# Optimization experiments

Hardware: AMD Instinct MI355X
Metric: run time of the kernel (lower is better)

The kernel has to match this reference:

```python
import jax, jax.numpy as jnp
import numpy as np

B, S, D = 2, 2048, 1024
H, DH = 16, 64
BS = 512            # block_size
MAX_LEN = 2048      # rope base = max_seq_length
NB = S // BS        # number of blocks (no padding: S % BS == 0)


def setup_inputs() -> dict:
    key = jax.random.key(0)
    ks = jax.random.split(key, 5)
    s = 1.0 / np.sqrt(D)
    x = jax.random.normal(ks[0], (B, S, D), jnp.float32)
    Wq = jax.random.normal(ks[1], (D, D), jnp.float32) * s
    Wk = jax.random.normal(ks[2], (D, D), jnp.float32) * s
    Wv = jax.random.normal(ks[3], (D, D), jnp.float32) * s
    Wo = jax.random.normal(ks[4], (D, D), jnp.float32) * s
    z = jnp.zeros((D,), jnp.float32)
    return {"x": x, "Wq": Wq, "bq": z, "Wk": Wk, "bk": z,
            "Wv": Wv, "bv": z, "Wo": Wo, "bo": z}


def _apply_rope(q, k):
    # inv_freq uses max_seq_length as the base (as in the source module)
    inv_freq = 1.0 / MAX_LEN ** (jnp.arange(0, DH, 2, dtype=jnp.float32) / DH)  # [DH/2]
    pos = jnp.arange(S, dtype=jnp.float32)
    freqs = jnp.outer(pos, inv_freq)                 # [S, DH/2]
    cos = jnp.cos(freqs)[None, :, None, :]           # [1,S,1,DH/2]
    sin = jnp.sin(freqs)[None, :, None, :]
    half = DH // 2
    q1, q2 = q[..., :half], q[..., half:]
    k1, k2 = k[..., :half], k[..., half:]
    q_rot = jnp.concatenate([q1 * cos - q2 * sin, q1 * sin + q2 * cos], axis=-1)
    k_rot = jnp.concatenate([k1 * cos - k2 * sin, k1 * sin + k2 * cos], axis=-1)
    return q_rot, k_rot


def _block_attn(qb, q_start, kb, vb, k_start):
    # qb,kb,vb: [B,H,BS,DH]; returns attended [B,H,BS,DH], lse [B,H,BS]
    scale = 1.0 / jnp.sqrt(DH)
    scores = jnp.einsum('bhqd,bhkd->bhqk', qb, kb) * scale
    q_pos = jnp.arange(BS) + q_start
    k_pos = jnp.arange(BS) + k_start
    mask = (q_pos[:, None] >= k_pos[None, :])[None, None]   # [1,1,BS,BS]
    scores = jnp.where(mask, scores, -1e9)
    mx = jnp.max(scores, axis=-1, keepdims=True)
    mx = jnp.where(jnp.isinf(mx), 0.0, mx)
    e = jnp.where(mask, jnp.exp(scores - mx), 0.0)
    se = jnp.sum(e, axis=-1, keepdims=True) + 1e-10
    attended = jnp.einsum('bhqk,bhkd->bhqd', e / se, vb)
    lse = (jnp.log(se) + mx)[..., 0]                        # [B,H,BS]
    return attended, lse


def _forward(x, Wq, bq, Wk, bk, Wv, bv, Wo, bo):
    q = (x @ Wq + bq).reshape(B, S, H, DH)
    k = (x @ Wk + bk).reshape(B, S, H, DH)
    v = (x @ Wv + bv).reshape(B, S, H, DH)
    q, k = _apply_rope(q, k)
    # split into blocks: [NB, B, H, BS, DH]
    def to_blocks(t):
        return t.reshape(B, NB, BS, H, DH).transpose(1, 0, 3, 2, 4)
    qb, kb, vb = to_blocks(q), to_blocks(k), to_blocks(v)
    starts = jnp.arange(NB) * BS
    inner = jax.vmap(_block_attn, in_axes=(None, None, 0, 0, 0))   # over k blocks
    outer = jax.vmap(inner, in_axes=(0, 0, None, None, None))      # over q blocks
    att, lse = outer(qb, starts, kb, vb, starts)
    # att: [NBq,NBk,B,H,BS,DH], lse: [NBq,NBk,B,H,BS]
    mlse = jnp.max(lse, axis=1, keepdims=True)
    w = jnp.exp(lse - mlse)
    w = w / (jnp.sum(w, axis=1, keepdims=True) + 1e-10)
    acc = jnp.sum(att * w[..., None], axis=1)                      # [NBq,B,H,BS,DH]
    out = acc.transpose(1, 0, 3, 2, 4).reshape(B, S, D)
    out = out @ Wo + bo
    return out


def reference(x, Wq, bq, Wk, bk, Wv, bv, Wo, bo):
    out = _forward(x, Wq, bq, Wk, bk, Wv, bv, Wo, bo)
    attention_weights = jnp.ones((B, H, S, S), jnp.float32)  # dummy, as in source
    return out, attention_weights
```

## Files before the change

kernel.cpp:

```cpp
#include <hip/hip_runtime.h>
#include <cstdint>
#include <cstddef>

#define DEVINL __device__ __forceinline__

typedef float   f32x4  __attribute__((ext_vector_type(4)));
typedef float   vf4    __attribute__((ext_vector_type(4)));
typedef __bf16  bf16x8 __attribute__((ext_vector_type(8)));
typedef uint32_t u32;
typedef unsigned short u16;
typedef uint32_t u32x4 __attribute__((ext_vector_type(4)));

constexpr int Bb = 2, Ss = 2048, Dd = 1024, Hh = 16;
constexpr int Mm = Bb * Ss;


DEVINL u16 f2bf(float f) {
  union { float f; u32 u; } a; a.f = f;
  u32 r = a.u + 0x7fffu + ((a.u >> 16) & 1u);
  return (u16)(r >> 16);
}

typedef const __attribute__((address_space(1))) void* gas_t;
typedef __attribute__((address_space(3))) void* las_t;
DEVINL void gld_lds16(const void* g, void* l) {
  __builtin_amdgcn_global_load_lds((gas_t)g, (las_t)l, 16, 0, 0);
}

__global__ void fill_ones(vf4* __restrict__ p, long long n4) {
  size_t i = (size_t)blockIdx.x * blockDim.x + threadIdx.x;
  size_t stride = (size_t)gridDim.x * blockDim.x;
  const vf4 one = {1.f, 1.f, 1.f, 1.f};
  for (; i < (size_t)n4; i += stride)
    __builtin_nontemporal_store(one, p + i);
}

__global__ void rope_table(float* __restrict__ cosT, float* __restrict__ sinT) {
  int idx = blockIdx.x * 256 + threadIdx.x;
  int s = idx >> 5, j = idx & 31;
  float freq = (float)s * exp2f(-11.0f * (float)j / 32.0f);
  cosT[idx] = cosf(freq);
  sinT[idx] = sinf(freq);
}

__global__ void cast_x(const float* __restrict__ x, u16* __restrict__ xb) {
  size_t i = ((size_t)blockIdx.x * 256 + threadIdx.x) * 4;
  vf4 v = *(const vf4*)(x + i);
  union { u16 u[4]; unsigned long long q; } o;
  o.u[0] = f2bf(v.x); o.u[1] = f2bf(v.y); o.u[2] = f2bf(v.z); o.u[3] = f2bf(v.w);
  *(unsigned long long*)(xb + i) = o.q;
}

__global__ void transpose_cast_W(const float* __restrict__ W0, const float* __restrict__ W1,
                                 const float* __restrict__ W2, const float* __restrict__ W3,
                                 u16* __restrict__ Wt) {
  __shared__ u16 tile[64][72];
  const int z = blockIdx.z;
  const float* W = (z == 0) ? W0 : (z == 1) ? W1 : (z == 2) ? W2 : W3;
  u16* Out = Wt + (size_t)z * (Dd * Dd);
  const int k0 = blockIdx.x * 64, n0 = blockIdx.y * 64;
  const int tid = threadIdx.x;
#pragma unroll
  for (int it = 0; it < 4; ++it) {
    int r = it * 16 + (tid >> 4);
    int c = (tid & 15) * 4;
    vf4 v = *(const vf4*)(W + (size_t)(k0 + r) * Dd + n0 + c);
    tile[r][c + 0] = f2bf(v.x); tile[r][c + 1] = f2bf(v.y);
    tile[r][c + 2] = f2bf(v.z); tile[r][c + 3] = f2bf(v.w);
  }
  __syncthreads();
#pragma unroll
  for (int it = 0; it < 2; ++it) {
    int c = it * 256 + tid;
    int n = c >> 3, ck = c & 7;
    union { u16 u[8]; u32x4 q; } o;
#pragma unroll
    for (int j = 0; j < 8; ++j) o.u[j] = tile[ck * 8 + j][n];
    *(u32x4*)(Out + (size_t)(n0 + n) * Dd + k0 + ck * 8) = o.q;
  }
}

DEVINL void gemm_mainloop(const u16* __restrict__ A, const u16* __restrict__ Bt,
                          int m0, int n0, char* lds, f32x4 (&acc)[4][4],
                          vf4* __restrict__ onesp, size_t obase) {
  const int tid = threadIdx.x, lane = tid & 63;
  const int w = tid >> 6, wr = w >> 1, wc = w & 1;
  const int l15 = lane & 15, l4 = lane >> 4;
  auto stage = [&](const u16* g, int row0, int k0, char* dst) {
#pragma unroll
    for (int h2 = 0; h2 < 2; ++h2) {
      int c = h2 * 256 + tid;
      const char* src = (const char*)g + (size_t)(row0 + (c >> 2)) * 2048 + k0 * 2 + (c & 3) * 16;
      gld_lds16(src, dst + c * 16);
    }
  };
  stage(A, m0, 0, lds);
  stage(Bt, n0, 0, lds + 16384);
  __syncthreads();
  const vf4 onev = {1.f, 1.f, 1.f, 1.f};
#pragma unroll 2
  for (int t = 0; t < 32; ++t) {
    const int cur = t & 1;
    char* As = lds + cur * 8192;
    char* Bs = lds + 16384 + cur * 8192;
    if (t < 31) {
      char* An = lds + (cur ^ 1) * 8192;
      char* Bn = lds + 16384 + (cur ^ 1) * 8192;
      stage(A, m0, (t + 1) * 32, An);
      stage(Bt, n0, (t + 1) * 32, Bn);
    }
    __builtin_nontemporal_store(onev, onesp + obase + (size_t)t * 512 + tid);
    __builtin_nontemporal_store(onev, onesp + obase + (size_t)t * 512 + 256 + tid);
    bf16x8 af[4], bfr[4];
#pragma unroll
    for (int mt = 0; mt < 4; ++mt)
      af[mt] = *(const bf16x8*)(As + (wr * 64 + mt * 16 + l15) * 64 + l4 * 16);
#pragma unroll
    for (int nt = 0; nt < 4; ++nt)
      bfr[nt] = *(const bf16x8*)(Bs + (wc * 64 + nt * 16 + l15) * 64 + l4 * 16);
#pragma unroll
    for (int mt = 0; mt < 4; ++mt)
#pragma unroll
      for (int nt = 0; nt < 4; ++nt)
        acc[mt][nt] = __builtin_amdgcn_mfma_f32_16x16x32_bf16(af[mt], bfr[nt], acc[mt][nt], 0, 0, 0);
    __syncthreads();
  }
}

template <int EPI>
__global__ __launch_bounds__(256) void gemm128(
    const u16* __restrict__ A, const u16* __restrict__ W0,
    const float* __restrict__ b0, const float* __restrict__ b1, const float* __restrict__ b2,
    const float* __restrict__ cosT, const float* __restrict__ sinT,
    u16* __restrict__ Qo, u16* __restrict__ Ko, u16* __restrict__ Vo,
    float* __restrict__ outp, vf4* __restrict__ onesp) {
  __shared__ __align__(16) char lds[32768];
  const int tid = threadIdx.x, lane = tid & 63;
  const int w = tid >> 6, wr = w >> 1, wc = w & 1;
  const int l15 = lane & 15, l4 = lane >> 4;

  const int lin = blockIdx.y * 32 + blockIdx.x;
  const int xcd = lin & 7, ix = lin >> 3;
  constexpr int YPX = (EPI == 0) ? 3 : 1;
  const int ytile = xcd * YPX + (ix >> 5);
  const int m0 = (ix & 31) * 128;

  int mat, n0;
  const u16* Bt;
  if (EPI == 0) { mat = ytile >> 3; n0 = (ytile & 7) * 128; Bt = W0 + (size_t)mat * (Dd * Dd); }
  else          { mat = 0;          n0 = ytile * 128;       Bt = W0; }
  const size_t obase = (EPI == 0 ? 0 : (size_t)12582912) + (size_t)lin * 16384;

  f32x4 acc[4][4] = {};
  gemm_mainloop(A, Bt, m0, n0, lds, acc, onesp, obase);

  if (EPI == 0) {
    const float* bias = (mat == 0) ? b0 : ((mat == 1) ? b1 : b2);
    u16* Out = (mat == 0) ? Qo : ((mat == 1) ? Ko : Vo);
    const bool dorope = (mat < 2);
#pragma unroll
    for (int mt = 0; mt < 4; ++mt) {
#pragma unroll
      for (int i = 0; i < 4; ++i) {
        int m = m0 + wr * 64 + mt * 16 + l4 * 4 + i;
        int bidx = m >> 11, s = m & 2047;
        float cv0 = 0.f, sv0 = 0.f, cv1 = 0.f, sv1 = 0.f;
        if (dorope) {
          cv0 = cosT[s * 32 + l15];      sv0 = sinT[s * 32 + l15];
          cv1 = cosT[s * 32 + 16 + l15]; sv1 = sinT[s * 32 + 16 + l15];
        }
#pragma unroll
        for (int nt = 0; nt < 4; ++nt) {
          int n = n0 + wc * 64 + nt * 16 + l15;
          float v = acc[mt][nt][i] + bias[n];
          float ov;
          if (dorope) {
            int np = n0 + wc * 64 + (nt ^ 2) * 16 + l15;
            float vp = acc[mt][nt ^ 2][i] + bias[np];
            float cc = (nt & 1) ? cv1 : cv0, sn = (nt & 1) ? sv1 : sv0;
            ov = (nt < 2) ? (v * cc - vp * sn)
                          : (vp * sn + v * cc);
          } else ov = v;
          int hh = n >> 6, dh = n & 63;
          Out[(((size_t)bidx * Hh + hh) * Ss + s) * 64 + dh] = f2bf(ov);
        }
      }
    }
  } else {
#pragma unroll
    for (int mt = 0; mt < 4; ++mt)
#pragma unroll
      for (int i = 0; i < 4; ++i) {
        int m = m0 + wr * 64 + mt * 16 + l4 * 4 + i;
#pragma unroll
        for (int nt = 0; nt < 4; ++nt) {
          int n = n0 + wc * 64 + nt * 16 + l15;
          outp[(size_t)m * Dd + n] = acc[mt][nt][i] + b0[n];
        }
      }
  }
}

__global__ void transpose_v(const u16* __restrict__ Vg, u16* __restrict__ Vtg) {
  __shared__ u16 tile[64][72];
  const int s0 = blockIdx.x * 64, bh = blockIdx.y;
  const int tid = threadIdx.x;
  const u16* Vb = Vg + (size_t)bh * Ss * 64;
  u16* Vtb = Vtg + (size_t)bh * 64 * Ss;
#pragma unroll
  for (int h2 = 0; h2 < 2; ++h2) {
    int c = h2 * 256 + tid;
    int r = c >> 3, ck = c & 7;
    u32x4 v = *(const u32x4*)(Vb + (size_t)(s0 + r) * 64 + ck * 8);
    const u16* t8 = (const u16*)&v;
#pragma unroll
    for (int j = 0; j < 8; ++j) tile[r][ck * 8 + j] = t8[j];
  }
  __syncthreads();
#pragma unroll
  for (int h2 = 0; h2 < 2; ++h2) {
    int c = h2 * 256 + tid;
    int dh = c >> 3, ck = c & 7;
    union { u16 u[8]; u32x4 q; } o;
#pragma unroll
    for (int j = 0; j < 8; ++j) o.u[j] = tile[ck * 8 + j][dh];
    *(u32x4*)(Vtb + (size_t)dh * Ss + s0 + ck * 8) = o.q;
  }
}

__global__ __launch_bounds__(256) void attn_kernel(
    const u16* __restrict__ Qg, const u16* __restrict__ Kg,
    const u16* __restrict__ Vtg, u16* __restrict__ Og) {
  __shared__ __align__(16) char lds[16384];

  const int tid = threadIdx.x, lane = tid & 63, w = tid >> 6;
  const int l15 = lane & 15, l4 = lane >> 4;

  const int bid = blockIdx.x;
  const int bh = bid & 31;
  const int qt_raw = (bid >> 5) & 7;
  const int qtile = (bid >> 8) ? qt_raw : (15 - qt_raw);
  const int qw = qtile * 128 + w * 32;
  const int tdiag = qw >> 6;

  const u16*  Qb  = Qg + (size_t)bh * Ss * 64;
  const char* Kb  = (const char*)(Kg + (size_t)bh * Ss * 64);
  const char* Vtb = (const char*)(Vtg + (size_t)bh * 64 * Ss);

  bf16x8 aq[2][2];
#pragma unroll
  for (int mt = 0; mt < 2; ++mt)
#pragma unroll
    for (int kt = 0; kt < 2; ++kt)
      aq[mt][kt] = *(const bf16x8*)(Qb + (size_t)(qw + mt * 16 + l15) * 64 + kt * 32 + l4 * 8);

  f32x4 accO[2][4] = {};
  float mrow[2][4], lrow[2][4];
#pragma unroll
  for (int mt = 0; mt < 2; ++mt)
#pragma unroll
    for (int i = 0; i < 4; ++i) { mrow[mt][i] = -1e30f; lrow[mt][i] = 0.f; }

  char* pw = lds + w * 4096;

  for (int t = 0; t <= tdiag; ++t) {
    const int kv0 = t * 64;

    f32x4 sf[2][4] = {};
#pragma unroll
    for (int kt = 0; kt < 2; ++kt) {
      bf16x8 bk[4];
#pragma unroll
      for (int nt = 0; nt < 4; ++nt)
        bk[nt] = *(const bf16x8*)(Kb + (size_t)(kv0 + nt * 16 + l15) * 128 + kt * 64 + l4 * 16);
      __builtin_amdgcn_s_setprio(1);
#pragma unroll
      for (int mt = 0; mt < 2; ++mt)
#pragma unroll
        for (int nt = 0; nt < 4; ++nt)
          sf[mt][nt] = __builtin_amdgcn_mfma_f32_16x16x32_bf16(aq[mt][kt], bk[nt], sf[mt][nt], 0, 0, 0);
      __builtin_amdgcn_s_setprio(0);
    }

    const bool diag = (t == tdiag);
#pragma unroll
    for (int mt = 0; mt < 2; ++mt) {
#pragma unroll
      for (int i = 0; i < 4; ++i) {
        int row = qw + mt * 16 + l4 * 4 + i;
        float sv[4];
        float mx = -1e30f;
#pragma unroll
        for (int nt = 0; nt < 4; ++nt) {
          float xv = sf[mt][nt][i] * 0.125f;
          if (diag && (kv0 + nt * 16 + l15) > row) xv = -1e30f;
          sv[nt] = xv; mx = fmaxf(mx, xv);
        }
        mx = fmaxf(mx, __shfl_xor(mx, 1));
        mx = fmaxf(mx, __shfl_xor(mx, 2));
        mx = fmaxf(mx, __shfl_xor(mx, 4));
        mx = fmaxf(mx, __shfl_xor(mx, 8));
        float mnew = fmaxf(mrow[mt][i], mx);
        float rescale = __expf(mrow[mt][i] - mnew);
        float rs = 0.f;
        int rl = mt * 16 + l4 * 4 + i;
#pragma unroll
        for (int nt = 0; nt < 4; ++nt) {
          float p = __expf(sv[nt] - mnew);
          rs += p;
          int key = nt * 16 + l15;
          int boff = rl * 128 + (((key >> 3) ^ (rl & 7)) << 4) + (key & 7) * 2;
          *(u16*)(pw + boff) = f2bf(p);
        }
        rs += __shfl_xor(rs, 1); rs += __shfl_xor(rs, 2);
        rs += __shfl_xor(rs, 4); rs += __shfl_xor(rs, 8);
        lrow[mt][i] = lrow[mt][i] * rescale + rs;
        mrow[mt][i] = mnew;
#pragma unroll
        for (int nt = 0; nt < 4; ++nt) accO[mt][nt][i] *= rescale;
      }
    }

#pragma unroll
    for (int ks = 0; ks < 2; ++ks) {
      bf16x8 ap[2], bv[4];
#pragma unroll
      for (int mt = 0; mt < 2; ++mt) {
        int row = mt * 16 + l15;
        int ch = (ks * 4 + l4) ^ (row & 7);
        ap[mt] = *(const bf16x8*)(pw + row * 128 + ch * 16);
      }
#pragma unroll
      for (int nt = 0; nt < 4; ++nt)
        bv[nt] = *(const bf16x8*)(Vtb + (size_t)(nt * 16 + l15) * (Ss * 2) + (size_t)kv0 * 2 + ks * 64 + l4 * 16);
      __builtin_amdgcn_s_setprio(1);
#pragma unroll
      for (int mt = 0; mt < 2; ++mt)
#pragma unroll
        for (int nt = 0; nt < 4; ++nt)
          accO[mt][nt] = __builtin_amdgcn_mfma_f32_16x16x32_bf16(ap[mt], bv[nt], accO[mt][nt], 0, 0, 0);
      __builtin_amdgcn_s_setprio(0);
    }
  }

  const int b = bh >> 4, h = bh & 15;
#pragma unroll
  for (int mt = 0; mt < 2; ++mt)
#pragma unroll
    for (int i = 0; i < 4; ++i) {
      int s = qw + mt * 16 + l4 * 4 + i;
      float inv = 1.0f / (lrow[mt][i] + 1e-10f);
      size_t rowbase = ((size_t)b * Ss + s) * Dd + h * 64;
#pragma unroll
      for (int nt = 0; nt < 4; ++nt)
        Og[rowbase + nt * 16 + l15] = f2bf(accO[mt][nt][i] * inv);
    }
}

extern "C" void kernel_launch(void* const* d_in, const int* in_sizes, int n_in,
                              void* d_out, int out_size, void* d_ws, size_t ws_size,
                              hipStream_t stream) {
  const float* x  = (const float*)d_in[0];
  const float* Wq = (const float*)d_in[1];
  const float* bq = (const float*)d_in[2];
  const float* Wk = (const float*)d_in[3];
  const float* bk = (const float*)d_in[4];
  const float* Wv = (const float*)d_in[5];
  const float* bv = (const float*)d_in[6];
  const float* Wo = (const float*)d_in[7];
  const float* bo = (const float*)d_in[8];
  float* out = (float*)d_out;

  char* ws = (char*)d_ws;
  u16*   xb   = (u16*)(ws);
  u16*   Wt   = (u16*)(ws + ((size_t)8 << 20));
  float* cosT = (float*)(ws + ((size_t)16 << 20));
  float* sinT = (float*)(ws + ((size_t)16 << 20) + ((size_t)256 << 10));
  u16*   Qg   = (u16*)(ws + ((size_t)17 << 20));
  u16*   Kg   = (u16*)(ws + ((size_t)25 << 20));
  u16*   Vg   = (u16*)(ws + ((size_t)33 << 20));
  u16*   Vtg  = (u16*)(ws + ((size_t)41 << 20));
  u16*   Og   = (u16*)(ws + ((size_t)49 << 20));

  size_t ones_off = (size_t)Mm * Dd;
  vf4* onesp = (vf4*)(out + ones_off);
  const long long n4_total = ((long long)out_size - (long long)ones_off) / 4;
  const long long n4_side  = 16777216;
  fill_ones<<<2048, 256, 0, stream>>>(onesp + n4_side, n4_total - n4_side);

  rope_table<<<256, 256, 0, stream>>>(cosT, sinT);
  cast_x<<<(Mm * Dd) / 1024, 256, 0, stream>>>(x, xb);
  transpose_cast_W<<<dim3(16, 16, 4), 256, 0, stream>>>(Wq, Wk, Wv, Wo, Wt);

  gemm128<0><<<dim3(32, 24), 256, 0, stream>>>(xb, Wt, bq, bk, bv, cosT, sinT,
                                               Qg, Kg, Vg, nullptr, onesp);
  transpose_v<<<dim3(32, 32), 256, 0, stream>>>(Vg, Vtg);
  attn_kernel<<<512, 256, 0, stream>>>(Qg, Kg, Vtg, Og);
  gemm128<1><<<dim3(32, 8), 256, 0, stream>>>(Og, Wt + (size_t)3 * Dd * Dd,
                                              bo, nullptr, nullptr, nullptr, nullptr,
                                              nullptr, nullptr, nullptr, out, onesp);
}
```

Baseline: 731.9 us.

## Spread dummy ones-fill across QKV GEMM, attention and smaller-tile output GEMM

```diff
diff --git a/kernel.cpp b/kernel.cpp
--- a/kernel.cpp
+++ b/kernel.cpp
@@ -13,7 +13,6 @@
 
 constexpr int Bb = 2, Ss = 2048, Dd = 1024, Hh = 16;
 constexpr int Mm = Bb * Ss;
-
 
 DEVINL u16 f2bf(float f) {
   union { float f; u32 u; } a; a.f = f;
@@ -80,46 +79,56 @@
   }
 }
 
+template <int BM>
 DEVINL void gemm_mainloop(const u16* __restrict__ A, const u16* __restrict__ Bt,
-                          int m0, int n0, char* lds, f32x4 (&acc)[4][4],
+                          int m0, int n0, char* lds, f32x4 (&acc)[BM / 32][4],
                           vf4* __restrict__ onesp, size_t obase) {
+  constexpr int MT = BM / 32;
+  constexpr int ABYTES = BM * 64;
   const int tid = threadIdx.x, lane = tid & 63;
   const int w = tid >> 6, wr = w >> 1, wc = w & 1;
   const int l15 = lane & 15, l4 = lane >> 4;
-  auto stage = [&](const u16* g, int row0, int k0, char* dst) {
+  char* Ab = lds;
+  char* Bb = lds + 2 * ABYTES;
+  auto stageA = [&](int k0, char* dst) {
+#pragma unroll
+    for (int h2 = 0; h2 < BM / 64; ++h2) {
+      int c = h2 * 256 + tid;
+      const char* src = (const char*)A + (size_t)(m0 + (c >> 2)) * 2048 + k0 * 2 + (c & 3) * 16;
+      gld_lds16(src, dst + c * 16);
+    }
+  };
+  auto stageB = [&](int k0, char* dst) {
 #pragma unroll
     for (int h2 = 0; h2 < 2; ++h2) {
       int c = h2 * 256 + tid;
-      const char* src = (const char*)g + (size_t)(row0 + (c >> 2)) * 2048 + k0 * 2 + (c & 3) * 16;
+      const char* src = (const char*)Bt + (size_t)(n0 + (c >> 2)) * 2048 + k0 * 2 + (c & 3) * 16;
       gld_lds16(src, dst + c * 16);
     }
   };
-  stage(A, m0, 0, lds);
-  stage(Bt, n0, 0, lds + 16384);
+  stageA(0, Ab);
+  stageB(0, Bb);
   __syncthreads();
   const vf4 onev = {1.f, 1.f, 1.f, 1.f};
 #pragma unroll 2
   for (int t = 0; t < 32; ++t) {
     const int cur = t & 1;
-    char* As = lds + cur * 8192;
-    char* Bs = lds + 16384 + cur * 8192;
+    char* As = Ab + cur * ABYTES;
+    char* Bs = Bb + cur * 8192;
     if (t < 31) {
-      char* An = lds + (cur ^ 1) * 8192;
-      char* Bn = lds + 16384 + (cur ^ 1) * 8192;
-      stage(A, m0, (t + 1) * 32, An);
-      stage(Bt, n0, (t + 1) * 32, Bn);
-    }
-    __builtin_nontemporal_store(onev, onesp + obase + (size_t)t * 512 + tid);
-    __builtin_nontemporal_store(onev, onesp + obase + (size_t)t * 512 + 256 + tid);
-    bf16x8 af[4], bfr[4];
-#pragma unroll
-    for (int mt = 0; mt < 4; ++mt)
-      af[mt] = *(const bf16x8*)(As + (wr * 64 + mt * 16 + l15) * 64 + l4 * 16);
+      stageA((t + 1) * 32, Ab + (cur ^ 1) * ABYTES);
+      stageB((t + 1) * 32, Bb + (cur ^ 1) * 8192);
+    }
+    __builtin_nontemporal_store(onev, onesp + obase + (size_t)t * 256 + tid);
+    bf16x8 af[MT], bfr[4];
+#pragma unroll
+    for (int mt = 0; mt < MT; ++mt)
+      af[mt] = *(const bf16x8*)(As + (wr * (MT * 16) + mt * 16 + l15) * 64 + l4 * 16);
 #pragma unroll
     for (int nt = 0; nt < 4; ++nt)
       bfr[nt] = *(const bf16x8*)(Bs + (wc * 64 + nt * 16 + l15) * 64 + l4 * 16);
 #pragma unroll
-    for (int mt = 0; mt < 4; ++mt)
+    for (int mt = 0; mt < MT; ++mt)
 #pragma unroll
       for (int nt = 0; nt < 4; ++nt)
         acc[mt][nt] = __builtin_amdgcn_mfma_f32_16x16x32_bf16(af[mt], bfr[nt], acc[mt][nt], 0, 0, 0);
@@ -134,35 +143,38 @@
     const float* __restrict__ cosT, const float* __restrict__ sinT,
     u16* __restrict__ Qo, u16* __restrict__ Ko, u16* __restrict__ Vo,
     float* __restrict__ outp, vf4* __restrict__ onesp) {
-  __shared__ __align__(16) char lds[32768];
+  constexpr int BM = (EPI == 0) ? 128 : 64;
+  constexpr int MT = BM / 32;
+  constexpr int MX = (EPI == 0) ? 32 : 64;
+  constexpr int YPX = (EPI == 0) ? 3 : 1;
+  __shared__ __align__(16) char lds[2 * BM * 64 + 16384];
   const int tid = threadIdx.x, lane = tid & 63;
   const int w = tid >> 6, wr = w >> 1, wc = w & 1;
   const int l15 = lane & 15, l4 = lane >> 4;
 
-  const int lin = blockIdx.y * 32 + blockIdx.x;
+  const int lin = blockIdx.y * MX + blockIdx.x;
   const int xcd = lin & 7, ix = lin >> 3;
-  constexpr int YPX = (EPI == 0) ? 3 : 1;
-  const int ytile = xcd * YPX + (ix >> 5);
-  const int m0 = (ix & 31) * 128;
+  const int ytile = xcd * YPX + ix / MX;
+  const int m0 = (ix % MX) * BM;
 
   int mat, n0;
   const u16* Bt;
   if (EPI == 0) { mat = ytile >> 3; n0 = (ytile & 7) * 128; Bt = W0 + (size_t)mat * (Dd * Dd); }
   else          { mat = 0;          n0 = ytile * 128;       Bt = W0; }
-  const size_t obase = (EPI == 0 ? 0 : (size_t)12582912) + (size_t)lin * 16384;
-
-  f32x4 acc[4][4] = {};
-  gemm_mainloop(A, Bt, m0, n0, lds, acc, onesp, obase);
+  const size_t obase = (EPI == 0 ? 0 : (size_t)6291456) + (size_t)lin * 8192;
+
+  f32x4 acc[MT][4] = {};
+  gemm_mainloop<BM>(A, Bt, m0, n0, lds, acc, onesp, obase);
 
   if (EPI == 0) {
     const float* bias = (mat == 0) ? b0 : ((mat == 1) ? b1 : b2);
     u16* Out = (mat == 0) ? Qo : ((mat == 1) ? Ko : Vo);
     const bool dorope = (mat < 2);
 #pragma unroll
-    for (int mt = 0; mt < 4; ++mt) {
+    for (int mt = 0; mt < MT; ++mt) {
 #pragma unroll
       for (int i = 0; i < 4; ++i) {
-        int m = m0 + wr * 64 + mt * 16 + l4 * 4 + i;
+        int m = m0 + wr * (MT * 16) + mt * 16 + l4 * 4 + i;
         int bidx = m >> 11, s = m & 2047;
         float cv0 = 0.f, sv0 = 0.f, cv1 = 0.f, sv1 = 0.f;
         if (dorope) {
@@ -188,10 +200,10 @@
     }
   } else {
 #pragma unroll
-    for (int mt = 0; mt < 4; ++mt)
+    for (int mt = 0; mt < MT; ++mt)
 #pragma unroll
       for (int i = 0; i < 4; ++i) {
-        int m = m0 + wr * 64 + mt * 16 + l4 * 4 + i;
+        int m = m0 + wr * (MT * 16) + mt * 16 + l4 * 4 + i;
 #pragma unroll
         for (int nt = 0; nt < 4; ++nt) {
           int n = n0 + wc * 64 + nt * 16 + l15;
@@ -230,7 +242,7 @@
 
 __global__ __launch_bounds__(256) void attn_kernel(
     const u16* __restrict__ Qg, const u16* __restrict__ Kg,
-    const u16* __restrict__ Vtg, u16* __restrict__ Og) {
+    const u16* __restrict__ Vtg, u16* __restrict__ Og, vf4* __restrict__ onesp) {
   __shared__ __align__(16) char lds[16384];
 
   const int tid = threadIdx.x, lane = tid & 63, w = tid >> 6;
@@ -243,6 +255,11 @@
   const int qw = qtile * 128 + w * 32;
   const int tdiag = qw >> 6;
 
+  const int quota = 2 * qtile + 1;
+  const size_t abase = (size_t)10485760 +
+      ((size_t)bh * 1024 + (size_t)(4 * qtile * qtile) + (size_t)w * quota) * 256 +
+      (size_t)lane * 4;
+
   const u16*  Qb  = Qg + (size_t)bh * Ss * 64;
   const char* Kb  = (const char*)(Kg + (size_t)bh * Ss * 64);
   const char* Vtb = (const char*)(Vtg + (size_t)bh * 64 * Ss);
@@ -262,9 +279,15 @@
     for (int i = 0; i < 4; ++i) { mrow[mt][i] = -1e30f; lrow[mt][i] = 0.f; }
 
   char* pw = lds + w * 4096;
+  const vf4 onev = {1.f, 1.f, 1.f, 1.f};
 
   for (int t = 0; t <= tdiag; ++t) {
     const int kv0 = t * 64;
+    if (t < quota) {
+#pragma unroll
+      for (int j = 0; j < 4; ++j)
+        __builtin_nontemporal_store(onev, onesp + abase + (size_t)t * 256 + j);
+    }
 
     f32x4 sf[2][4] = {};
 #pragma unroll
@@ -385,7 +408,7 @@
   size_t ones_off = (size_t)Mm * Dd;
   vf4* onesp = (vf4*)(out + ones_off);
   const long long n4_total = ((long long)out_size - (long long)ones_off) / 4;
-  const long long n4_side  = 16777216;
+  const long long n4_side  = 18874368;
   fill_ones<<<2048, 256, 0, stream>>>(onesp + n4_side, n4_total - n4_side);
 
   rope_table<<<256, 256, 0, stream>>>(cosT, sinT);
@@ -395,8 +418,8 @@
   gemm128<0><<<dim3(32, 24), 256, 0, stream>>>(xb, Wt, bq, bk, bv, cosT, sinT,
                                                Qg, Kg, Vg, nullptr, onesp);
   transpose_v<<<dim3(32, 32), 256, 0, stream>>>(Vg, Vtg);
-  attn_kernel<<<512, 256, 0, stream>>>(Qg, Kg, Vtg, Og);
-  gemm128<1><<<dim3(32, 8), 256, 0, stream>>>(Og, Wt + (size_t)3 * Dd * Dd,
+  attn_kernel<<<512, 256, 0, stream>>>(Qg, Kg, Vtg, Og, onesp);
+  gemm128<1><<<dim3(64, 8), 256, 0, stream>>>(Og, Wt + (size_t)3 * Dd * Dd,
                                               bo, nullptr, nullptr, nullptr, nullptr,
                                               nullptr, nullptr, nullptr, out, onesp);
 }
```

Result: no change. 733.8 us (+0.3%).
